# Kernel optimization log

Hardware: AMD Instinct MI355X
Metric: run time of the kernel (lower is better)

Reference implementation:

```python
import jax, jax.numpy as jnp
import numpy as np

B, T, C = 4, 2048, 2048
H, KV, HD = 16, 4, 128  # n_head, n_kv_head, head_dim
G = H // KV             # query heads per kv head


def _rope(t, cos, sin):
    # t: [B, T, h, HD]; cos/sin: [T, HD//2] -> broadcast as [1, T, 1, HD//2]
    tr = t.reshape(t.shape[:-1] + (HD // 2, 2))
    t_r, t_i = tr[..., 0], tr[..., 1]
    c = cos[None, :, None, :]
    s = sin[None, :, None, :]
    o_r = t_r * c - t_i * s
    o_i = t_r * s + t_i * c
    return jnp.stack((o_r, o_i), axis=-1).reshape(t.shape)


def setup_inputs() -> dict:
    key = jax.random.key(0)
    ks = jax.random.split(key, 7)
    sc = 0.02
    return {
        "x": jax.random.normal(ks[0], (B, T, C), jnp.float32),
        "cos_freqs": jnp.cos(jnp.outer(jnp.arange(T, dtype=jnp.float32),
                                       1.0 / (10000.0 ** (jnp.arange(HD // 2, dtype=jnp.float32) * 2 / HD)))),
        "sin_freqs": jnp.sin(jnp.outer(jnp.arange(T, dtype=jnp.float32),
                                       1.0 / (10000.0 ** (jnp.arange(HD // 2, dtype=jnp.float32) * 2 / HD)))),
        "wq": jax.random.normal(ks[1], (H * HD, C), jnp.float32) * sc,
        "wk": jax.random.normal(ks[2], (KV * HD, C), jnp.float32) * sc,
        "wv": jax.random.normal(ks[3], (KV * HD, C), jnp.float32) * sc,
        "wo": jax.random.normal(ks[4], (C, H * HD), jnp.float32) * sc,
    }


def reference(x, cos_freqs, sin_freqs, wq, wk, wv, wo):
    # projections (Linear with bias=False: y = x @ W.T)
    q = (x @ wq.T).reshape(B, T, H, HD)
    k = (x @ wk.T).reshape(B, T, KV, HD)
    v = (x @ wv.T).reshape(B, T, KV, HD)
    q, k = _rope(q, cos_freqs, sin_freqs), _rope(k, cos_freqs, sin_freqs)
    # GQA attention without materializing repeated K/V: group q heads per kv head
    qg = q.reshape(B, T, KV, G, HD).transpose(0, 2, 3, 1, 4)  # [B,KV,G,T,HD]
    kh = k.transpose(0, 2, 1, 3)                              # [B,KV,T,HD]
    vh = v.transpose(0, 2, 1, 3)                              # [B,KV,T,HD]
    scale = 1.0 / jnp.sqrt(jnp.float32(HD))
    scores = jnp.einsum('bkgtd,bksd->bkgts', qg, kh) * scale  # [B,KV,G,T,T]
    mask = jnp.tril(jnp.ones((T, T), dtype=bool))
    scores = jnp.where(mask, scores, jnp.float32(-jnp.inf))
    attn = jax.nn.softmax(scores, axis=-1)
    out = jnp.einsum('bkgts,bksd->bkgtd', attn, vh)           # [B,KV,G,T,HD]
    out = out.transpose(0, 3, 1, 2, 4).reshape(B, T, H * HD)
    return out @ wo.T
```

## Files before the change

### kernel.cpp

```cpp
#include <hip/hip_runtime.h>
#include <hip/hip_bf16.h>
#include <math.h>

typedef __attribute__((ext_vector_type(8))) short short8;
typedef __attribute__((ext_vector_type(4))) float floatx4;

__device__ __forceinline__ float bf2f(unsigned short u) {
  union { unsigned int i; float f; } x; x.i = ((unsigned int)u) << 16; return x.f;
}
__device__ __forceinline__ unsigned short f2bf(float f) {
  union { float f; unsigned int i; } x; x.f = f;
  unsigned int r = x.i + 0x7FFFu + ((x.i >> 16) & 1u);
  return (unsigned short)(r >> 16);
}
__device__ __forceinline__ unsigned int pack2bf(float a, float b) {
  return (unsigned int)f2bf(a) | ((unsigned int)f2bf(b) << 16);
}
__device__ __forceinline__ void gl16(const void* g, void* l) {
  __builtin_amdgcn_global_load_lds(
      (const __attribute__((address_space(1))) unsigned int*)g,
      (__attribute__((address_space(3))) unsigned int*)l, 16, 0, 0);
}

__global__ void cvt_f32_bf16(const float* __restrict__ in, unsigned short* __restrict__ out, int n4) {
  int i = blockIdx.x * blockDim.x + threadIdx.x;
  if (i >= n4) return;
  float4 v = ((const float4*)in)[i];
  ushort4 o;
  o.x = f2bf(v.x); o.y = f2bf(v.y); o.z = f2bf(v.z); o.w = f2bf(v.w);
  ((ushort4*)out)[i] = o;
}

template<int MODE>
__global__ __launch_bounds__(512, 2) void gemm_bt(const unsigned short* __restrict__ A,
                                                  const unsigned short* __restrict__ Bw,
                                                  void* __restrict__ out0,
                                                  unsigned short* __restrict__ vtg,
                                                  int M, int N, int K, int nbx) {
  __shared__ __align__(16) unsigned short SM[32768];
  const int nb = gridDim.x;
  const int bid = blockIdx.x;
  const int tile = (bid & 7) * (nb >> 3) + (bid >> 3);
  const int n0 = (tile % nbx) * 256, m0 = (tile / nbx) * 256;
  const int tid = threadIdx.x;
  const int lane = tid & 63, wave = tid >> 6;
  const int wm = wave >> 2, wn = wave & 3;
  const int r = lane & 15, g = lane >> 4;
  const int swzr = (r >> 1) & 3;

  const int scg = (tid & 3) ^ ((tid >> 3) & 3);
  const unsigned short* Ag0 = A  + (size_t)(m0 + (tid >> 2)) * K + scg * 8;
  const unsigned short* Bg0 = Bw + (size_t)(n0 + (tid >> 2)) * K + scg * 8;
  const size_t K128 = (size_t)K * 128;
  char* const SMb = (char*)SM;

  const int aoff = wm * 4096 + r * 32 + ((g ^ swzr) << 3);
  const int boff = 16384 + (wn >> 1) * 4096 + ((wn & 1) * 64 + r) * 32 + ((g ^ swzr) << 3);

  auto STAGE = [&](int s, int t) {
    const size_t ko = (size_t)t << 5;
    char* dA = SMb + s * 16384 + wave * 1024;
    char* dB = SMb + 32768 + s * 16384 + wave * 1024;
    gl16(Ag0 + ko,        dA);
    gl16(Ag0 + K128 + ko, dA + 8192);
    gl16(Bg0 + ko,        dB);
    gl16(Bg0 + K128 + ko, dB + 8192);
  };

  floatx4 acc[8][4] = {};
  const int NT = K >> 5;

  STAGE(0, 0);
  STAGE(1, 1);
  asm volatile("s_waitcnt vmcnt(4)" ::: "memory");
  __builtin_amdgcn_s_barrier();
  asm volatile("" ::: "memory");

  for (int t = 0; t < NT; ++t) {
    const int s = t & 1;
    const unsigned short* Ls = SM + s * 8192;

    short8 bfr[4];
#pragma unroll
    for (int j = 0; j < 4; ++j) bfr[j] = *(const short8*)&Ls[boff + j * 512];
    short8 af0 = *(const short8*)&Ls[aoff];
    short8 af1 = *(const short8*)&Ls[aoff + 512];
    __builtin_amdgcn_s_barrier();
    asm volatile("" ::: "memory");
    __builtin_amdgcn_s_setprio(1);
#pragma unroll
    for (int j = 0; j < 4; ++j) {
      acc[0][j] = __builtin_amdgcn_mfma_f32_16x16x32_bf16(af0, bfr[j], acc[0][j], 0, 0, 0);
      acc[1][j] = __builtin_amdgcn_mfma_f32_16x16x32_bf16(af1, bfr[j], acc[1][j], 0, 0, 0);
    }
    __builtin_amdgcn_s_setprio(0);

    short8 af2 = *(const short8*)&Ls[aoff + 2 * 512];
    short8 af3 = *(const short8*)&Ls[aoff + 3 * 512];
    __builtin_amdgcn_s_barrier();
    asm volatile("" ::: "memory");
    __builtin_amdgcn_s_setprio(1);
#pragma unroll
    for (int j = 0; j < 4; ++j) {
      acc[2][j] = __builtin_amdgcn_mfma_f32_16x16x32_bf16(af2, bfr[j], acc[2][j], 0, 0, 0);
      acc[3][j] = __builtin_amdgcn_mfma_f32_16x16x32_bf16(af3, bfr[j], acc[3][j], 0, 0, 0);
    }
    __builtin_amdgcn_s_setprio(0);

    short8 af4 = *(const short8*)&Ls[aoff + 4 * 512];
    short8 af5 = *(const short8*)&Ls[aoff + 5 * 512];
    __builtin_amdgcn_s_barrier();
    asm volatile("" ::: "memory");
    __builtin_amdgcn_s_setprio(1);
#pragma unroll
    for (int j = 0; j < 4; ++j) {
      acc[4][j] = __builtin_amdgcn_mfma_f32_16x16x32_bf16(af4, bfr[j], acc[4][j], 0, 0, 0);
      acc[5][j] = __builtin_amdgcn_mfma_f32_16x16x32_bf16(af5, bfr[j], acc[5][j], 0, 0, 0);
    }
    __builtin_amdgcn_s_setprio(0);

    short8 af6 = *(const short8*)&Ls[aoff + 6 * 512];
    short8 af7 = *(const short8*)&Ls[aoff + 7 * 512];
    asm volatile("s_waitcnt lgkmcnt(0)" ::: "memory");
    __builtin_amdgcn_sched_barrier(0);
    __builtin_amdgcn_s_barrier();
    asm volatile("" ::: "memory");
    if (t + 2 < NT) {
      STAGE(s, t + 2);
      asm volatile("s_waitcnt vmcnt(4)" ::: "memory");
    } else if (t + 1 < NT) {
      asm volatile("s_waitcnt vmcnt(0)" ::: "memory");
    }
    __builtin_amdgcn_s_barrier();
    asm volatile("" ::: "memory");
    __builtin_amdgcn_s_setprio(1);
#pragma unroll
    for (int j = 0; j < 4; ++j) {
      acc[6][j] = __builtin_amdgcn_mfma_f32_16x16x32_bf16(af6, bfr[j], acc[6][j], 0, 0, 0);
      acc[7][j] = __builtin_amdgcn_mfma_f32_16x16x32_bf16(af7, bfr[j], acc[7][j], 0, 0, 0);
    }
    __builtin_amdgcn_s_setprio(0);
  }

  if (MODE == 0) {
    float* SMf = (float*)SM;
    float* outp = (float*)out0;
#pragma unroll
    for (int sp = 0; sp < 4; ++sp) {
      __syncthreads();
      if (wn == sp) {
#pragma unroll
        for (int i = 0; i < 8; ++i)
#pragma unroll
          for (int j = 0; j < 4; ++j)
#pragma unroll
            for (int q = 0; q < 4; ++q)
              SMf[(wm * 128 + i * 16 + g * 4 + q) * 64 + j * 16 + r] = acc[i][j][q];
      }
      __syncthreads();
#pragma unroll
      for (int it = 0; it < 8; ++it) {
        int c = it * 512 + tid;
        int ml = c >> 4, c4 = c & 15;
        float4 v = *(float4*)&SMf[ml * 64 + c4 * 4];
        *(float4*)(outp + (size_t)(m0 + ml) * N + n0 + sp * 64 + c4 * 4) = v;
      }
    }
  } else if (n0 < 2560) {
    unsigned short* outp = (unsigned short*)out0;
#pragma unroll
    for (int sp = 0; sp < 2; ++sp) {
      __syncthreads();
      if (wm == sp) {
#pragma unroll
        for (int i = 0; i < 8; ++i)
#pragma unroll
          for (int j = 0; j < 4; ++j)
#pragma unroll
            for (int q = 0; q < 4; ++q)
              SM[(i * 16 + g * 4 + q) * 256 + wn * 64 + j * 16 + r] = f2bf(acc[i][j][q]);
      }
      __syncthreads();
#pragma unroll
      for (int it = 0; it < 8; ++it) {
        int c = it * 512 + tid;
        int ml = c >> 5, c8 = c & 31;
        short8 v = *(short8*)&SM[ml * 256 + c8 * 8];
        *(short8*)(outp + (size_t)(m0 + sp * 128 + ml) * N + n0 + c8 * 8) = v;
      }
    }
  } else {
#pragma unroll
    for (int sp = 0; sp < 8; ++sp) {
      __syncthreads();
      if (wave == sp) {
#pragma unroll
        for (int i = 0; i < 8; ++i)
#pragma unroll
          for (int j = 0; j < 4; ++j)
#pragma unroll
            for (int q = 0; q < 4; ++q) {
              int ml = i * 16 + g * 4 + q;
              int nl = j * 16 + r;
              SM[nl * 128 + (((ml >> 3) ^ (nl & 7)) << 3) + (ml & 7)] = f2bf(acc[i][j][q]);
            }
      }
      __syncthreads();
#pragma unroll
      for (int it = 0; it < 2; ++it) {
        int c = it * 512 + tid;
        int nl = c >> 4, m8 = c & 15;
        short8 v = *(short8*)&SM[nl * 128 + ((m8 ^ (nl & 7)) << 3)];
        *(short8*)(vtg + (size_t)(n0 - 2560 + (sp & 3) * 64 + nl) * 8192 + m0 + (sp >> 2) * 128 + m8 * 8) = v;
      }
    }
  }
}

__global__ void rope_inplace(unsigned short* __restrict__ t,
                             const float* __restrict__ cosf, const float* __restrict__ sinf,
                             int heads, int rowStride, int total, float scale) {
  int i = blockIdx.x * blockDim.x + threadIdx.x;
  if (i >= total) return;
  int d8 = i & 15;
  int rem = i >> 4;
  int head = rem % heads;
  int tok = rem / heads;
  int tpos = tok & 2047;
  unsigned short* p = t + (size_t)tok * rowStride + head * 128 + d8 * 8;
  short8 v = *(short8*)p;
  float4 c = *(const float4*)(cosf + (size_t)tpos * 64 + d8 * 4);
  float4 s = *(const float4*)(sinf + (size_t)tpos * 64 + d8 * 4);
  float cc[4] = {c.x, c.y, c.z, c.w};
  float ss[4] = {s.x, s.y, s.z, s.w};
  short8 o;
#pragma unroll
  for (int j = 0; j < 4; ++j) {
    float tr = bf2f((unsigned short)v[2 * j]);
    float ti = bf2f((unsigned short)v[2 * j + 1]);
    float orr = (tr * cc[j] - ti * ss[j]) * scale;
    float oi  = (tr * ss[j] + ti * cc[j]) * scale;
    o[2 * j]     = (short)f2bf(orr);
    o[2 * j + 1] = (short)f2bf(oi);
  }
  *(short8*)p = o;
}

__global__ __launch_bounds__(256, 2) void attn_fwd(const unsigned short* __restrict__ QKV,
                                                   const unsigned short* __restrict__ VT,
                                                   unsigned short* __restrict__ O) {
  constexpr int T = 2048;
  constexpr int LDQ = 3072;
  constexpr float NEG = -1e30f;
  __shared__ unsigned short Ks[2][64 * 128];
  __shared__ unsigned short Vs[2][128 * 64];
  const int gid = blockIdx.x;
  const int hb  = gid & 63;
  const int p   = gid >> 6;
  const int h = hb & 15, b = hb >> 4;
  const int kvh = h >> 2;
  const int tid = threadIdx.x, lane = tid & 63, w = tid >> 6;
  const int r = lane & 15, g = lane >> 4;
  const int rbase = (r & 3) + ((r >> 2) << 3);
  const int swzr  = (r & 3) | (((r >> 2) & 1) << 2);
  const size_t bT = (size_t)b * T;

  const unsigned short* Kgb = QKV + bT * LDQ + 2048 + kvh * 128;
  const unsigned short* Vgb = VT + (size_t)(kvh * 128) * 8192 + b * 2048;

  auto STAGE = [&](int bi, int kv0) {
#pragma unroll
    for (int t2 = 0; t2 < 4; ++t2) {
      int ck = w * 4 + t2;
      { int row = ck * 4 + (lane >> 4); int c16 = lane & 15;
        int swz = (row & 3) | (((row >> 3) & 1) << 2);
        gl16(Kgb + (size_t)(kv0 + row) * LDQ + ((c16 ^ swz) << 3),
             (char*)(&Ks[bi][0]) + ck * 1024); }
      { int row = ck * 8 + (lane >> 3); int c16 = lane & 7;
        gl16(Vgb + (size_t)row * 8192 + kv0 + ((c16 ^ (row & 7)) << 3),
             (char*)(&Vs[bi][0]) + ck * 1024); }
    }
  };

  for (int seg = 0; seg < 2; ++seg) {
    const int qb = seg ? p : 15 - p;
    const int q0 = qb * 128;

    short8 qf[2][4];
#pragma unroll
    for (int qt = 0; qt < 2; ++qt) {
      const unsigned short* qp = QKV + (bT + q0 + w * 32 + qt * 16 + r) * LDQ + h * 128;
#pragma unroll
      for (int c = 0; c < 4; ++c) qf[qt][c] = *(const short8*)(qp + c * 32 + g * 8);
    }

    floatx4 acc[8][2] = {};
    float mrun[2] = {NEG, NEG};
    float lrun[2] = {0.f, 0.f};

    const int ntiles = (q0 + 128) >> 6;
    STAGE(0, 0);
    asm volatile("s_waitcnt vmcnt(0)" ::: "memory");
    __syncthreads();

    for (int t = 0; t < ntiles; ++t) {
      const int cur = t & 1;
      const int kv0 = t << 6;
      if (t + 1 < ntiles) STAGE(cur ^ 1, (t + 1) << 6);

      if (kv0 <= q0 + w * 32 + 31) {
        floatx4 st[2][4] = {};
        __builtin_amdgcn_s_setprio(1);
#pragma unroll
        for (int c = 0; c < 4; ++c) {
          short8 kf[4];
#pragma unroll
          for (int kt = 0; kt < 4; ++kt) {
            const int row = rbase + ((kt & 1) << 2) + ((kt >> 1) << 5);
            kf[kt] = *(const short8*)&Ks[cur][row * 128 + (((g + 4 * c) ^ swzr) << 3)];
          }
#pragma unroll
          for (int qt = 0; qt < 2; ++qt)
#pragma unroll
            for (int kt = 0; kt < 4; ++kt)
              st[qt][kt] = __builtin_amdgcn_mfma_f32_16x16x32_bf16(kf[kt], qf[qt][c], st[qt][kt], 0, 0, 0);
        }
        __builtin_amdgcn_s_setprio(0);

        short8 va[2][8];
#pragma unroll
        for (int kc = 0; kc < 2; ++kc)
#pragma unroll
          for (int dt = 0; dt < 8; ++dt)
            va[kc][dt] = *(const short8*)&Vs[cur][(dt * 16 + r) * 64 + (((g + 4 * kc) ^ (r & 7)) << 3)];

#pragma unroll
        for (int qt = 0; qt < 2; ++qt) {
          const int qmin = q0 + w * 32 + qt * 16;
          const int qrow = qmin + r;
          float x[4][4];
          bool needmask = (kv0 + 64 > qmin);
#pragma unroll
          for (int kt = 0; kt < 4; ++kt) {
            const int kvb = kv0 + ((kt >> 1) << 5) + (g << 3) + ((kt & 1) << 2);
#pragma unroll
            for (int j = 0; j < 4; ++j) {
              float v = st[qt][kt][j];
              if (needmask) v = (kvb + j <= qrow) ? v : NEG;
              x[kt][j] = v;
            }
          }
          float mloc = x[0][0];
#pragma unroll
          for (int kt = 0; kt < 4; ++kt)
#pragma unroll
            for (int j = 0; j < 4; ++j) mloc = fmaxf(mloc, x[kt][j]);
          mloc = fmaxf(mloc, __shfl_xor(mloc, 16));
          mloc = fmaxf(mloc, __shfl_xor(mloc, 32));
          if (!__all(mloc <= mrun[qt] + 8.f)) {
            float mnew = fmaxf(mrun[qt], mloc);
            float al = __expf(mrun[qt] - mnew);
            mrun[qt] = mnew;
            lrun[qt] *= al;
#pragma unroll
            for (int dt = 0; dt < 8; ++dt) acc[dt][qt] *= al;
          }
          float pr[4][4], ssum = 0.f;
#pragma unroll
          for (int kt = 0; kt < 4; ++kt)
#pragma unroll
            for (int j = 0; j < 4; ++j) { pr[kt][j] = __expf(x[kt][j] - mrun[qt]); ssum += pr[kt][j]; }
          ssum += __shfl_xor(ssum, 16);
          ssum += __shfl_xor(ssum, 32);
          lrun[qt] += ssum;
          uint2 pk[4];
#pragma unroll
          for (int kt = 0; kt < 4; ++kt) {
            pk[kt].x = pack2bf(pr[kt][0], pr[kt][1]);
            pk[kt].y = pack2bf(pr[kt][2], pr[kt][3]);
          }
          __builtin_amdgcn_s_setprio(1);
#pragma unroll
          for (int kc = 0; kc < 2; ++kc) {
            union { unsigned int u[4]; short8 s; } bw;
            bw.u[0] = pk[2 * kc].x;
            bw.u[1] = pk[2 * kc].y;
            bw.u[2] = pk[2 * kc + 1].x;
            bw.u[3] = pk[2 * kc + 1].y;
#pragma unroll
            for (int dt = 0; dt < 8; ++dt)
              acc[dt][qt] = __builtin_amdgcn_mfma_f32_16x16x32_bf16(va[kc][dt], bw.s, acc[dt][qt], 0, 0, 0);
          }
          __builtin_amdgcn_s_setprio(0);
        }
      }

      asm volatile("s_waitcnt vmcnt(0)" ::: "memory");
      __syncthreads();
    }

#pragma unroll
    for (int qt = 0; qt < 2; ++qt) {
      float inv = 1.f / lrun[qt];
      unsigned short* op = O + (bT + q0 + w * 32 + qt * 16 + r) * 2048 + h * 128;
#pragma unroll
      for (int dt = 0; dt < 8; ++dt) {
        uint2 pkd;
        pkd.x = pack2bf(acc[dt][qt][0] * inv, acc[dt][qt][1] * inv);
        pkd.y = pack2bf(acc[dt][qt][2] * inv, acc[dt][qt][3] * inv);
        *(uint2*)(op + dt * 16 + g * 4) = pkd;
      }
    }
  }
}

extern "C" void kernel_launch(void* const* d_in, const int* in_sizes, int n_in,
                              void* d_out, int out_size, void* d_ws, size_t ws_size,
                              hipStream_t stream) {
  const float* x    = (const float*)d_in[0];
  const float* cosf = (const float*)d_in[1];
  const float* sinf = (const float*)d_in[2];
  const float* wq   = (const float*)d_in[3];
  const float* wk   = (const float*)d_in[4];
  const float* wv   = (const float*)d_in[5];
  const float* wo   = (const float*)d_in[6];

  unsigned short* xb   = (unsigned short*)d_ws;
  unsigned short* qkvw = xb   + 16777216;
  unsigned short* wob  = qkvw + 6291456;
  unsigned short* qkv  = wob  + 4194304;
  unsigned short* Vtg  = qkv  + 25165824;
  unsigned short* AO   = Vtg  + 4194304;

  cvt_f32_bf16<<<16384, 256, 0, stream>>>(x,  xb,  4194304);
  cvt_f32_bf16<<<4096,  256, 0, stream>>>(wq, qkvw,           1048576);
  cvt_f32_bf16<<<1024,  256, 0, stream>>>(wk, qkvw + 4194304, 262144);
  cvt_f32_bf16<<<1024,  256, 0, stream>>>(wv, qkvw + 5242880, 262144);
  cvt_f32_bf16<<<4096,  256, 0, stream>>>(wo, wob, 1048576);

  gemm_bt<1><<<384, 512, 0, stream>>>(xb, qkvw, qkv, Vtg, 8192, 3072, 2048, 12);

  rope_inplace<<<8192, 256, 0, stream>>>(qkv,        cosf, sinf, 16, 3072, 2097152, 0.08838834764831845f);
  rope_inplace<<<2048, 256, 0, stream>>>(qkv + 2048, cosf, sinf, 4,  3072, 524288,  1.0f);

  attn_fwd<<<512, 256, 0, stream>>>(qkv, Vtg, AO);

  gemm_bt<0><<<256, 512, 0, stream>>>(AO, wob, d_out, nullptr, 8192, 2048, 2048, 8);
}
```

Measured before the change: 371.1 us.

## Triple-buffer GEMM LDS stages and split A/B prefetch across the k-loop

Moves the bf16 GEMM from a two-stage to a three-stage shared-memory ring (96 KB dynamic LDS) and issues the A and B tile prefetches at separate points inside each k-step. It also cuts the per-iteration barriers from five to two and drops the explicit lgkmcnt wait, grouping MFMAs into two halves of 16. The aim is to overlap global loads with compute better and reduce barrier stalls. The cost is more LDS per block, which may lower how many blocks fit per CU, and the mixed A/B staging timing around the vmcnt waits needs to stay correct.

```diff
diff --git a/kernel.cpp b/kernel.cpp
--- a/kernel.cpp
+++ b/kernel.cpp
@@ -37,7 +37,7 @@
                                                   void* __restrict__ out0,
                                                   unsigned short* __restrict__ vtg,
                                                   int M, int N, int K, int nbx) {
-  __shared__ __align__(16) unsigned short SM[32768];
+  extern __shared__ unsigned short SM[];
   const int nb = gridDim.x;
   const int bid = blockIdx.x;
   const int tile = (bid & 7) * (nb >> 3) + (bid >> 3);
@@ -54,15 +54,18 @@
   const size_t K128 = (size_t)K * 128;
   char* const SMb = (char*)SM;
 
-  const int aoff = wm * 4096 + r * 32 + ((g ^ swzr) << 3);
-  const int boff = 16384 + (wn >> 1) * 4096 + ((wn & 1) * 64 + r) * 32 + ((g ^ swzr) << 3);
-
-  auto STAGE = [&](int s, int t) {
+  const int aoff0 = (wm * 128 + r) * 32 + ((g ^ swzr) << 3);
+  const int boff0 = 8192 + (wn * 64 + r) * 32 + ((g ^ swzr) << 3);
+
+  auto STAGE_A = [&](int s, int t) {
     const size_t ko = (size_t)t << 5;
-    char* dA = SMb + s * 16384 + wave * 1024;
-    char* dB = SMb + 32768 + s * 16384 + wave * 1024;
+    char* dA = SMb + s * 32768 + wave * 1024;
     gl16(Ag0 + ko,        dA);
     gl16(Ag0 + K128 + ko, dA + 8192);
+  };
+  auto STAGE_B = [&](int s, int t) {
+    const size_t ko = (size_t)t << 5;
+    char* dB = SMb + s * 32768 + 16384 + wave * 1024;
     gl16(Bg0 + ko,        dB);
     gl16(Bg0 + K128 + ko, dB + 8192);
   };
@@ -70,76 +73,53 @@
   floatx4 acc[8][4] = {};
   const int NT = K >> 5;
 
-  STAGE(0, 0);
-  STAGE(1, 1);
+  STAGE_A(0, 0); STAGE_B(0, 0);
+  STAGE_A(1, 1); STAGE_B(1, 1);
   asm volatile("s_waitcnt vmcnt(4)" ::: "memory");
   __builtin_amdgcn_s_barrier();
   asm volatile("" ::: "memory");
 
+  int rd = 0, st = 2;
   for (int t = 0; t < NT; ++t) {
-    const int s = t & 1;
-    const unsigned short* Ls = SM + s * 8192;
-
-    short8 bfr[4];
-#pragma unroll
-    for (int j = 0; j < 4; ++j) bfr[j] = *(const short8*)&Ls[boff + j * 512];
-    short8 af0 = *(const short8*)&Ls[aoff];
-    short8 af1 = *(const short8*)&Ls[aoff + 512];
+    const unsigned short* Ls = SM + rd * 16384;
+    const bool pf = (t + 2 < NT);
+
+    short8 bfr[4], af[8];
+#pragma unroll
+    for (int j = 0; j < 4; ++j) bfr[j] = *(const short8*)&Ls[boff0 + j * 512];
+#pragma unroll
+    for (int i = 0; i < 4; ++i) af[i] = *(const short8*)&Ls[aoff0 + i * 512];
+    if (pf) STAGE_A(st, t + 2);
+    __builtin_amdgcn_s_barrier();
+    asm volatile("" ::: "memory");
+#pragma unroll
+    for (int i = 4; i < 8; ++i) af[i] = *(const short8*)&Ls[aoff0 + i * 512];
+    __builtin_amdgcn_s_setprio(1);
+#pragma unroll
+    for (int i = 0; i < 4; ++i)
+#pragma unroll
+      for (int j = 0; j < 4; ++j)
+        acc[i][j] = __builtin_amdgcn_mfma_f32_16x16x32_bf16(af[i], bfr[j], acc[i][j], 0, 0, 0);
+    __builtin_amdgcn_s_setprio(0);
+
+    if (pf) {
+      STAGE_B(st, t + 2);
+      asm volatile("s_waitcnt vmcnt(4)" ::: "memory");
+    } else {
+      asm volatile("s_waitcnt vmcnt(0)" ::: "memory");
+    }
     __builtin_amdgcn_s_barrier();
     asm volatile("" ::: "memory");
     __builtin_amdgcn_s_setprio(1);
 #pragma unroll
-    for (int j = 0; j < 4; ++j) {
-      acc[0][j] = __builtin_amdgcn_mfma_f32_16x16x32_bf16(af0, bfr[j], acc[0][j], 0, 0, 0);
-      acc[1][j] = __builtin_amdgcn_mfma_f32_16x16x32_bf16(af1, bfr[j], acc[1][j], 0, 0, 0);
-    }
+    for (int i = 4; i < 8; ++i)
+#pragma unroll
+      for (int j = 0; j < 4; ++j)
+        acc[i][j] = __builtin_amdgcn_mfma_f32_16x16x32_bf16(af[i], bfr[j], acc[i][j], 0, 0, 0);
     __builtin_amdgcn_s_setprio(0);
 
-    short8 af2 = *(const short8*)&Ls[aoff + 2 * 512];
-    short8 af3 = *(const short8*)&Ls[aoff + 3 * 512];
-    __builtin_amdgcn_s_barrier();
-    asm volatile("" ::: "memory");
-    __builtin_amdgcn_s_setprio(1);
-#pragma unroll
-    for (int j = 0; j < 4; ++j) {
-      acc[2][j] = __builtin_amdgcn_mfma_f32_16x16x32_bf16(af2, bfr[j], acc[2][j], 0, 0, 0);
-      acc[3][j] = __builtin_amdgcn_mfma_f32_16x16x32_bf16(af3, bfr[j], acc[3][j], 0, 0, 0);
-    }
-    __builtin_amdgcn_s_setprio(0);
-
-    short8 af4 = *(const short8*)&Ls[aoff + 4 * 512];
-    short8 af5 = *(const short8*)&Ls[aoff + 5 * 512];
-    __builtin_amdgcn_s_barrier();
-    asm volatile("" ::: "memory");
-    __builtin_amdgcn_s_setprio(1);
-#pragma unroll
-    for (int j = 0; j < 4; ++j) {
-      acc[4][j] = __builtin_amdgcn_mfma_f32_16x16x32_bf16(af4, bfr[j], acc[4][j], 0, 0, 0);
-      acc[5][j] = __builtin_amdgcn_mfma_f32_16x16x32_bf16(af5, bfr[j], acc[5][j], 0, 0, 0);
-    }
-    __builtin_amdgcn_s_setprio(0);
-
-    short8 af6 = *(const short8*)&Ls[aoff + 6 * 512];
-    short8 af7 = *(const short8*)&Ls[aoff + 7 * 512];
-    asm volatile("s_waitcnt lgkmcnt(0)" ::: "memory");
-    __builtin_amdgcn_sched_barrier(0);
-    __builtin_amdgcn_s_barrier();
-    asm volatile("" ::: "memory");
-    if (t + 2 < NT) {
-      STAGE(s, t + 2);
-      asm volatile("s_waitcnt vmcnt(4)" ::: "memory");
-    } else if (t + 1 < NT) {
-      asm volatile("s_waitcnt vmcnt(0)" ::: "memory");
-    }
-    __builtin_amdgcn_s_barrier();
-    asm volatile("" ::: "memory");
-    __builtin_amdgcn_s_setprio(1);
-#pragma unroll
-    for (int j = 0; j < 4; ++j) {
-      acc[6][j] = __builtin_amdgcn_mfma_f32_16x16x32_bf16(af6, bfr[j], acc[6][j], 0, 0, 0);
-      acc[7][j] = __builtin_amdgcn_mfma_f32_16x16x32_bf16(af7, bfr[j], acc[7][j], 0, 0, 0);
-    }
-    __builtin_amdgcn_s_setprio(0);
+    rd = (rd == 2) ? 0 : rd + 1;
+    st = (st == 2) ? 0 : st + 1;
   }
 
   if (MODE == 0) {
@@ -432,18 +412,25 @@
   unsigned short* Vtg  = qkv  + 25165824;
   unsigned short* AO   = Vtg  + 4194304;
 
+  static int _attr_once = []() {
+    hipFuncSetAttribute((const void*)gemm_bt<0>, hipFuncAttributeMaxDynamicSharedMemorySize, 98304);
+    hipFuncSetAttribute((const void*)gemm_bt<1>, hipFuncAttributeMaxDynamicSharedMemorySize, 98304);
+    return 0;
+  }();
+  (void)_attr_once;
+
   cvt_f32_bf16<<<16384, 256, 0, stream>>>(x,  xb,  4194304);
   cvt_f32_bf16<<<4096,  256, 0, stream>>>(wq, qkvw,           1048576);
   cvt_f32_bf16<<<1024,  256, 0, stream>>>(wk, qkvw + 4194304, 262144);
   cvt_f32_bf16<<<1024,  256, 0, stream>>>(wv, qkvw + 5242880, 262144);
   cvt_f32_bf16<<<4096,  256, 0, stream>>>(wo, wob, 1048576);
 
-  gemm_bt<1><<<384, 512, 0, stream>>>(xb, qkvw, qkv, Vtg, 8192, 3072, 2048, 12);
+  gemm_bt<1><<<384, 512, 98304, stream>>>(xb, qkvw, qkv, Vtg, 8192, 3072, 2048, 12);
 
   rope_inplace<<<8192, 256, 0, stream>>>(qkv,        cosf, sinf, 16, 3072, 2097152, 0.08838834764831845f);
   rope_inplace<<<2048, 256, 0, stream>>>(qkv + 2048, cosf, sinf, 4,  3072, 524288,  1.0f);
 
   attn_fwd<<<512, 256, 0, stream>>>(qkv, Vtg, AO);
 
-  gemm_bt<0><<<256, 512, 0, stream>>>(AO, wob, d_out, nullptr, 8192, 2048, 2048, 8);
-}
+  gemm_bt<0><<<256, 512, 98304, stream>>>(AO, wob, d_out, nullptr, 8192, 2048, 2048, 8);
+}
```

Measured after the change: 369.2 us. No clear change (-0.5%).
